# Performance work log

Measured on AMD Instinct MI355X. Metric: run time of the kernel, lower is better.

## Reference

```python
import jax, jax.numpy as jnp
import numpy as np

BATCH, NODES, ENC, DEC = 8192, 1_000_000, 128, 128


def setup_inputs() -> dict:
    key = jax.random.key(0)
    k1, k2, k3, k4 = jax.random.split(key, 4)
    query = jax.random.normal(k1, (BATCH, DEC), dtype=jnp.float32)
    values = jax.random.normal(k2, (NODES, ENC), dtype=jnp.float32)
    index = jax.random.randint(k3, (NODES,), 0, BATCH)
    W = jax.random.uniform(k4, (DEC, ENC), dtype=jnp.float32)
    return {"query": query, "values": values, "index": index, "W": W}


def reference(query, values, index, W):
    # query: [B, Ddec], values: [N, Denc], index: [N] in [0, B), W: [Ddec, Denc]
    batch = query.shape[0]
    dec = W.shape[0]
    # Original computes scores = query @ (W @ values.T) -> [B, N], then
    # scatter_softmax per segment along nodes, then gathers weights[index[n], n].
    # Only the row index[n] of column n is ever used, so we compute exactly
    # those entries: s[n] = <query[index[n]] @ W, values[n]> / sqrt(dec).
    qW = query @ W                                   # [B, Denc]
    s = jnp.einsum("ne,ne->n", qW[index], values)    # [N]
    s = s / jnp.sqrt(jnp.asarray(dec, dtype=s.dtype))
    # segment-wise stable softmax over nodes within each segment
    smax = jax.ops.segment_max(s, index, num_segments=batch)   # [B]
    e = jnp.exp(s - smax[index])                               # [N]
    denom = jax.ops.segment_sum(e, index, num_segments=batch)  # [B]
    w = e / denom[index]                                       # [N]
    # weighted scatter-add pooling -> [B, Denc]
    return jax.ops.segment_sum(w[:, None] * values, index, num_segments=batch)
```

## Files before the change

### kernel.cpp

```cpp
#include <hip/hip_runtime.h>
#include <cmath>

#define ENCD 128
#define DECD 128
#define INV_SQRT_D 0.08838834764831845f

__global__ void init_counts(int* __restrict__ counts, int B) {
    int i = blockIdx.x * blockDim.x + threadIdx.x;
    if (i < B) counts[i] = 0;
}

__global__ void qw_gemm(const float* __restrict__ query, const float* __restrict__ W,
                        float* __restrict__ qW) {
    __shared__ float qs[8][DECD];
    const int t = threadIdx.x;
    const int row0 = blockIdx.x * 8;
    for (int i = t; i < 8 * DECD; i += 256)
        qs[i >> 7][i & 127] = query[(size_t)row0 * DECD + i];
    __syncthreads();
    const int c = t & 127;
    const int rh = t >> 7;
    float a0 = 0.f, a1 = 0.f, a2 = 0.f, a3 = 0.f;
    for (int k = 0; k < DECD; ++k) {
        const float w = W[k * ENCD + c];
        a0 += qs[rh * 4 + 0][k] * w;
        a1 += qs[rh * 4 + 1][k] * w;
        a2 += qs[rh * 4 + 2][k] * w;
        a3 += qs[rh * 4 + 3][k] * w;
    }
    qW[(size_t)(row0 + rh * 4 + 0) * ENCD + c] = a0;
    qW[(size_t)(row0 + rh * 4 + 1) * ENCD + c] = a1;
    qW[(size_t)(row0 + rh * 4 + 2) * ENCD + c] = a2;
    qW[(size_t)(row0 + rh * 4 + 3) * ENCD + c] = a3;
}

__global__ void hist_kernel(const int* __restrict__ index, int* __restrict__ counts, int N) {
    int n4 = (blockIdx.x * blockDim.x + threadIdx.x) * 4;
    if (n4 + 3 < N) {
        const int4 v = *(const int4*)(index + n4);
        atomicAdd(&counts[v.x], 1);
        atomicAdd(&counts[v.y], 1);
        atomicAdd(&counts[v.z], 1);
        atomicAdd(&counts[v.w], 1);
    } else {
        for (int n = n4; n < N; ++n) atomicAdd(&counts[index[n]], 1);
    }
}

__global__ void scan_kernel(const int* __restrict__ counts, int* __restrict__ offsets,
                            int* __restrict__ cursor, int B) {
    __shared__ int tot[1024];
    const int t = threadIdx.x;
    int local[8];
    int s = 0;
#pragma unroll
    for (int i = 0; i < 8; ++i) {
        const int ci = t * 8 + i;
        local[i] = (ci < B) ? counts[ci] : 0;
        s += local[i];
    }
    tot[t] = s;
    __syncthreads();
    for (int off = 1; off < 1024; off <<= 1) {
        int v = (t >= off) ? tot[t - off] : 0;
        __syncthreads();
        tot[t] += v;
        __syncthreads();
    }
    int excl = tot[t] - s;
#pragma unroll
    for (int i = 0; i < 8; ++i) {
        const int ci = t * 8 + i;
        if (ci < B) { offsets[ci] = excl; cursor[ci] = excl; }
        excl += local[i];
    }
    if (t == 1023) offsets[B] = tot[1023];
}

__global__ void scatter_kernel(const int* __restrict__ index, int* __restrict__ cursor,
                               int* __restrict__ nodeids, int N) {
    int n4 = (blockIdx.x * blockDim.x + threadIdx.x) * 4;
    if (n4 + 3 < N) {
        const int4 v = *(const int4*)(index + n4);
        const int p0 = atomicAdd(&cursor[v.x], 1); nodeids[p0] = n4 + 0;
        const int p1 = atomicAdd(&cursor[v.y], 1); nodeids[p1] = n4 + 1;
        const int p2 = atomicAdd(&cursor[v.z], 1); nodeids[p2] = n4 + 2;
        const int p3 = atomicAdd(&cursor[v.w], 1); nodeids[p3] = n4 + 3;
    } else {
        for (int n = n4; n < N; ++n) {
            const int p = atomicAdd(&cursor[index[n]], 1);
            nodeids[p] = n;
        }
    }
}

__device__ __forceinline__ float dot4(const float4 a, const float4 b) {
    return a.x * b.x + a.y * b.y + a.z * b.z + a.w * b.w;
}

#define SEG_ITER(CUR, NXT, P)                                                  \
  {                                                                            \
    float pd = dot4(CUR[0], q4[0]) + dot4(CUR[1], q4[1]) +                     \
               dot4(CUR[2], q4[2]) + dot4(CUR[3], q4[3]);                      \
    pd += __shfl_xor(pd, 8);                                                   \
    pd += __shfl_xor(pd, 16);                                                  \
    pd += __shfl_xor(pd, 32);                                                  \
    const float sc = ((P) + r < end) ? pd * INV_SQRT_D : -INFINITY;            \
    float mc = sc;                                                             \
    mc = fmaxf(mc, __shfl_xor(mc, 1));                                         \
    mc = fmaxf(mc, __shfl_xor(mc, 2));                                         \
    mc = fmaxf(mc, __shfl_xor(mc, 4));                                         \
    const float m_new = fmaxf(m, mc);      \
    const float scale = __expf(m - m_new);        \
    const float pe = __expf(sc - m_new);        \
    float* dst = &vsh[w][r][g * 16];                                           \
    *(float4*)(dst + 0)  = CUR[0];                                             \
    *(float4*)(dst + 4)  = CUR[1];                                             \
    *(float4*)(dst + 8)  = CUR[2];                                             \
    *(float4*)(dst + 12) = CUR[3];                                             \
    if ((P) + 32 < end) {                              \
      const float* vp = values + (size_t)nid_next * ENCD + g * 16;             \
      NXT[0] = *(const float4*)(vp + 0);                                       \
      NXT[1] = *(const float4*)(vp + 4);                                       \
      NXT[2] = *(const float4*)(vp + 8);                                       \
      NXT[3] = *(const float4*)(vp + 12);                                      \
      const int nn = (P) + 64 + r;                                             \
      nid_next = nodeids[(nn < end) ? nn : beg];                               \
    }                                                                          \
    float psum = 0.f, ad0 = 0.f, ad1 = 0.f;                                    \
    _Pragma("unroll")                                                          \
    for (int j = 0; j < 8; ++j) {                                              \
      const float pj = __shfl(pe, j);           \
      psum += pj;                                                              \
      ad0 += pj * vsh[w][j][l];        \
      ad1 += pj * vsh[w][j][l + 64];                                           \
    }                                                                          \
    acc0 = acc0 * scale + ad0;                                                 \
    acc1 = acc1 * scale + ad1;                                                 \
    lacc = lacc * scale + psum;                                                \
    m = m_new;                                                                 \
  }

__global__ __launch_bounds__(256) void seg_attn(
    const float* __restrict__ values, const float* __restrict__ qW,
    const int* __restrict__ offsets, const int* __restrict__ nodeids,
    float* __restrict__ out) {
    const int b = blockIdx.x;
    const int t = threadIdx.x;
    const int w = t >> 6;
    const int l = t & 63;
    const int r = l & 7;
    const int g = l >> 3;

    const int beg = offsets[b];
    const int end = offsets[b + 1];

    __shared__ float vsh[4][8][ENCD + 4];
    __shared__ float mrg_a[4][ENCD];
    __shared__ float mrg_l[4];
    __shared__ float mrg_m[4];

    float4 q4[4];
#pragma unroll
    for (int i = 0; i < 4; ++i)
        q4[i] = *(const float4*)(qW + (size_t)b * ENCD + g * 16 + i * 4);

    float acc0 = 0.f, acc1 = 0.f, lacc = 0.f;
    float m = -INFINITY;
    float4 va[4], vb[4];
    int nid_next = 0;

    int p = beg + w * 8;
    if (p < end) {
        {
            const int pp = p + r;
            const int nid0 = nodeids[(pp < end) ? pp : beg];
            const float* vp = values + (size_t)nid0 * ENCD + g * 16;
            va[0] = *(const float4*)(vp + 0);
            va[1] = *(const float4*)(vp + 4);
            va[2] = *(const float4*)(vp + 8);
            va[3] = *(const float4*)(vp + 12);
            const int np = p + 32 + r;
            nid_next = nodeids[(np < end) ? np : beg];
        }
        while (true) {
            SEG_ITER(va, vb, p);
            p += 32;
            if (p >= end) break;
            SEG_ITER(vb, va, p);
            p += 32;
            if (p >= end) break;
        }
    }

    mrg_a[w][l] = acc0;
    mrg_a[w][l + 64] = acc1;
    if (l == 0) { mrg_l[w] = lacc; mrg_m[w] = m; }
    __syncthreads();
    if (t < ENCD) {
        const float mt = fmaxf(fmaxf(mrg_m[0], mrg_m[1]), fmaxf(mrg_m[2], mrg_m[3]));
        float a = 0.f, lt = 0.f;
#pragma unroll
        for (int ww = 0; ww < 4; ++ww) {
            const float mw = mrg_m[ww];
            const float rs = (mw == mt) ? 1.f : __expf(mw - mt);
            a += rs * mrg_a[ww][t];
            lt += rs * mrg_l[ww];
        }
        out[(size_t)b * ENCD + t] = (lt > 0.f) ? (a / lt) : 0.f;
    }
}

extern "C" void kernel_launch(void* const* d_in, const int* in_sizes, int n_in,
                              void* d_out, int out_size, void* d_ws, size_t ws_size,
                              hipStream_t stream) {
    const float* query  = (const float*)d_in[0];
    const float* values = (const float*)d_in[1];
    const int*   index  = (const int*)d_in[2];
    const float* W      = (const float*)d_in[3];
    float* out = (float*)d_out;

    const int B = in_sizes[0] / DECD;
    const int N = in_sizes[2];

    float* qW      = (float*)d_ws;
    int*   nodeids = (int*)(qW + (size_t)B * ENCD);
    int*   counts  = nodeids + N;
    int*   offsets = counts + B;
    int*   cursor  = offsets + B + 1;

    init_counts<<<(B + 255) / 256, 256, 0, stream>>>(counts, B);
    qw_gemm<<<B / 8, 256, 0, stream>>>(query, W, qW);
    hist_kernel<<<(N / 4 + 255) / 256, 256, 0, stream>>>(index, counts, N);
    scan_kernel<<<1, 1024, 0, stream>>>(counts, offsets, cursor, B);
    scatter_kernel<<<(N / 4 + 255) / 256, 256, 0, stream>>>(index, cursor, nodeids, N);
    seg_attn<<<B, 256, 0, stream>>>(values, qW, offsets, nodeids, out);
}
```

Before: 833.2 us.

## Map one wavefront per segment with register accumulation instead of shared-memory pooling

The segment attention kernel now gives each 64-lane wavefront its own segment, so four segments share a block instead of one segment being split across four waves and merged through shared memory. Each lane keeps 16 accumulator columns in registers and applies the online-softmax rescale only when the running max grows. The shared-memory staging of value rows and the per-node shuffle broadcast are dropped, and the 8 node-groups are reduced with shuffles once at the end. Costs: more registers per lane, less parallelism within each segment, and lanes inside a wave may be unevenly loaded because segment lengths vary.

```diff
diff --git a/kernel.cpp b/kernel.cpp
--- a/kernel.cpp
+++ b/kernel.cpp
@@ -102,112 +102,113 @@
   {                                                                            \
     float pd = dot4(CUR[0], q4[0]) + dot4(CUR[1], q4[1]) +                     \
                dot4(CUR[2], q4[2]) + dot4(CUR[3], q4[3]);                      \
-    pd += __shfl_xor(pd, 8);                                                   \
-    pd += __shfl_xor(pd, 16);                                                  \
-    pd += __shfl_xor(pd, 32);                                                  \
+    pd += __shfl_xor(pd, 1);                    \
+    pd += __shfl_xor(pd, 2);                                                   \
+    pd += __shfl_xor(pd, 4);                                                   \
     const float sc = ((P) + r < end) ? pd * INV_SQRT_D : -INFINITY;            \
-    float mc = sc;                                                             \
-    mc = fmaxf(mc, __shfl_xor(mc, 1));                                         \
-    mc = fmaxf(mc, __shfl_xor(mc, 2));                                         \
-    mc = fmaxf(mc, __shfl_xor(mc, 4));                                         \
-    const float m_new = fmaxf(m, mc);      \
-    const float scale = __expf(m - m_new);        \
-    const float pe = __expf(sc - m_new);        \
-    float* dst = &vsh[w][r][g * 16];                                           \
-    *(float4*)(dst + 0)  = CUR[0];                                             \
-    *(float4*)(dst + 4)  = CUR[1];                                             \
-    *(float4*)(dst + 8)  = CUR[2];                                             \
-    *(float4*)(dst + 12) = CUR[3];                                             \
-    if ((P) + 32 < end) {                              \
-      const float* vp = values + (size_t)nid_next * ENCD + g * 16;             \
+    float mc = sc;               \
+    mc = fmaxf(mc, __shfl_xor(mc, 8));                                         \
+    mc = fmaxf(mc, __shfl_xor(mc, 16));                                        \
+    mc = fmaxf(mc, __shfl_xor(mc, 32));                                        \
+    if (mc > m) {                  \
+      const float scale = __expf(m - mc);         \
+      _Pragma("unroll")                                                        \
+      for (int i = 0; i < 16; ++i) acc[i] *= scale;                            \
+      lacc *= scale;                                                           \
+      m = mc;                                                                  \
+    }                                                                          \
+    const float pe = __expf(sc - m);            \
+    if ((P) + 8 < end) {                      \
+      const float* vp = values + (size_t)nid_next * ENCD + g4;                 \
       NXT[0] = *(const float4*)(vp + 0);                                       \
-      NXT[1] = *(const float4*)(vp + 4);                                       \
-      NXT[2] = *(const float4*)(vp + 8);                                       \
-      NXT[3] = *(const float4*)(vp + 12);                                      \
-      const int nn = (P) + 64 + r;                                             \
+      NXT[1] = *(const float4*)(vp + 32);                                      \
+      NXT[2] = *(const float4*)(vp + 64);                                      \
+      NXT[3] = *(const float4*)(vp + 96);                                      \
+      const int nn = (P) + 16 + r;                                             \
       nid_next = nodeids[(nn < end) ? nn : beg];                               \
     }                                                                          \
-    float psum = 0.f, ad0 = 0.f, ad1 = 0.f;                                    \
     _Pragma("unroll")                                                          \
-    for (int j = 0; j < 8; ++j) {                                              \
-      const float pj = __shfl(pe, j);           \
-      psum += pj;                                                              \
-      ad0 += pj * vsh[w][j][l];        \
-      ad1 += pj * vsh[w][j][l + 64];                                           \
+    for (int i = 0; i < 4; ++i) {  \
+      acc[i * 4 + 0] += pe * CUR[i].x;                                         \
+      acc[i * 4 + 1] += pe * CUR[i].y;                                         \
+      acc[i * 4 + 2] += pe * CUR[i].z;                                         \
+      acc[i * 4 + 3] += pe * CUR[i].w;                                         \
     }                                                                          \
-    acc0 = acc0 * scale + ad0;                                                 \
-    acc1 = acc1 * scale + ad1;                                                 \
-    lacc = lacc * scale + psum;                                                \
-    m = m_new;                                                                 \
+    lacc += pe;                                                                \
   }
 
 __global__ __launch_bounds__(256) void seg_attn(
     const float* __restrict__ values, const float* __restrict__ qW,
     const int* __restrict__ offsets, const int* __restrict__ nodeids,
     float* __restrict__ out) {
-    const int b = blockIdx.x;
     const int t = threadIdx.x;
     const int w = t >> 6;
+    const int b = blockIdx.x * 4 + w;
     const int l = t & 63;
-    const int r = l & 7;
-    const int g = l >> 3;
+    const int r = l >> 3;
+    const int g4 = (l & 7) * 4;
 
     const int beg = offsets[b];
     const int end = offsets[b + 1];
 
-    __shared__ float vsh[4][8][ENCD + 4];
-    __shared__ float mrg_a[4][ENCD];
-    __shared__ float mrg_l[4];
-    __shared__ float mrg_m[4];
-
     float4 q4[4];
-#pragma unroll
-    for (int i = 0; i < 4; ++i)
-        q4[i] = *(const float4*)(qW + (size_t)b * ENCD + g * 16 + i * 4);
-
-    float acc0 = 0.f, acc1 = 0.f, lacc = 0.f;
+    const float* qp = qW + (size_t)b * ENCD + g4;
+    q4[0] = *(const float4*)(qp + 0);
+    q4[1] = *(const float4*)(qp + 32);
+    q4[2] = *(const float4*)(qp + 64);
+    q4[3] = *(const float4*)(qp + 96);
+
+    float acc[16];
+#pragma unroll
+    for (int i = 0; i < 16; ++i) acc[i] = 0.f;
+    float lacc = 0.f;
     float m = -INFINITY;
     float4 va[4], vb[4];
     int nid_next = 0;
 
-    int p = beg + w * 8;
+    int p = beg;
     if (p < end) {
-        {
-            const int pp = p + r;
-            const int nid0 = nodeids[(pp < end) ? pp : beg];
-            const float* vp = values + (size_t)nid0 * ENCD + g * 16;
-            va[0] = *(const float4*)(vp + 0);
-            va[1] = *(const float4*)(vp + 4);
-            va[2] = *(const float4*)(vp + 8);
-            va[3] = *(const float4*)(vp + 12);
-            const int np = p + 32 + r;
-            nid_next = nodeids[(np < end) ? np : beg];
-        }
+        const int pp = p + r;
+        const int nid0 = nodeids[(pp < end) ? pp : beg];
+        const float* vp = values + (size_t)nid0 * ENCD + g4;
+        va[0] = *(const float4*)(vp + 0);
+        va[1] = *(const float4*)(vp + 32);
+        va[2] = *(const float4*)(vp + 64);
+        va[3] = *(const float4*)(vp + 96);
+        const int np = p + 8 + r;
+        nid_next = nodeids[(np < end) ? np : beg];
         while (true) {
             SEG_ITER(va, vb, p);
-            p += 32;
+            p += 8;
             if (p >= end) break;
             SEG_ITER(vb, va, p);
-            p += 32;
+            p += 8;
             if (p >= end) break;
         }
     }
 
-    mrg_a[w][l] = acc0;
-    mrg_a[w][l + 64] = acc1;
-    if (l == 0) { mrg_l[w] = lacc; mrg_m[w] = m; }
-    __syncthreads();
-    if (t < ENCD) {
-        const float mt = fmaxf(fmaxf(mrg_m[0], mrg_m[1]), fmaxf(mrg_m[2], mrg_m[3]));
-        float a = 0.f, lt = 0.f;
-#pragma unroll
-        for (int ww = 0; ww < 4; ++ww) {
-            const float mw = mrg_m[ww];
-            const float rs = (mw == mt) ? 1.f : __expf(mw - mt);
-            a += rs * mrg_a[ww][t];
-            lt += rs * mrg_l[ww];
+#pragma unroll
+    for (int i = 0; i < 16; ++i) {
+        acc[i] += __shfl_xor(acc[i], 8);
+        acc[i] += __shfl_xor(acc[i], 16);
+        acc[i] += __shfl_xor(acc[i], 32);
+    }
+    lacc += __shfl_xor(lacc, 8);
+    lacc += __shfl_xor(lacc, 16);
+    lacc += __shfl_xor(lacc, 32);
+
+    if (r == 0) {
+        const float inv = (lacc > 0.f) ? 1.f / lacc : 0.f;
+        float* op = out + (size_t)b * ENCD + g4;
+#pragma unroll
+        for (int i = 0; i < 4; ++i) {
+            float4 o;
+            o.x = acc[i * 4 + 0] * inv;
+            o.y = acc[i * 4 + 1] * inv;
+            o.z = acc[i * 4 + 2] * inv;
+            o.w = acc[i * 4 + 3] * inv;
+            *(float4*)(op + i * 32) = o;
         }
-        out[(size_t)b * ENCD + t] = (lt > 0.f) ? (a / lt) : 0.f;
     }
 }
 
@@ -234,5 +235,5 @@
     hist_kernel<<<(N / 4 + 255) / 256, 256, 0, stream>>>(index, counts, N);
     scan_kernel<<<1, 1024, 0, stream>>>(counts, offsets, cursor, B);
     scatter_kernel<<<(N / 4 + 255) / 256, 256, 0, stream>>>(index, cursor, nodeids, N);
-    seg_attn<<<B, 256, 0, stream>>>(values, qW, offsets, nodeids, out);
-}
+    seg_attn<<<B / 4, 256, 0, stream>>>(values, qW, offsets, nodeids, out);
+}
```

After: 838.8 us. About the same (+0.7%).
